# Kernel optimization log

Measured on AMD Instinct MI355X. Metric: run time of the kernel, lower is better.

The kernel has to match this reference:

```python
import jax, jax.numpy as jnp
import numpy as np

B, T, D = 8, 8192, 256
H = 16            # history_length
K = 3             # neighbor kernel_size
DECAY = 0.9
EPS = 1e-5


def _layernorm(x, g, b):
    m = jnp.mean(x, axis=-1, keepdims=True)
    v = jnp.var(x, axis=-1, keepdims=True)
    return (x - m) * jax.lax.rsqrt(v + EPS) * g + b


def _window_weighted_sum(x_pad, weights, seq_len):
    # sum_j w[j] * x_pad[:, j:j+T, :] -- fixed-weight local aggregation,
    # avoids materializing the [B,T,W,D] unfold tensor.
    out = weights[0] * x_pad[:, 0:seq_len, :]
    for j in range(1, weights.shape[0]):
        out = out + weights[j] * x_pad[:, j:j + seq_len, :]
    return out


def temporal_weights():
    w = DECAY ** np.arange(H, dtype=np.float32)
    return jnp.asarray(w / w.sum())


def setup_inputs() -> dict:
    key = jax.random.key(0)
    ks = jax.random.split(key, 16)
    s = 1.0 / np.sqrt(D)
    s2 = 1.0 / np.sqrt(2 * D)
    inp = {
        "x": jax.random.normal(ks[0], (B, T, D), jnp.float32),
        # LayerNorms
        "n1_g": jnp.ones((D,), jnp.float32), "n1_b": jnp.zeros((D,), jnp.float32),
        "n2_g": jnp.ones((D,), jnp.float32), "n2_b": jnp.zeros((D,), jnp.float32),
        "n3_g": jnp.ones((D,), jnp.float32), "n3_b": jnp.zeros((D,), jnp.float32),
        # temporal value/out proj (stored as [in,out])
        "t_Wv": jax.random.uniform(ks[1], (D, D), jnp.float32, -s, s),
        "t_bv": jax.random.uniform(ks[2], (D,), jnp.float32, -s, s),
        "t_Wo": jax.random.uniform(ks[3], (D, D), jnp.float32, -s, s),
        "t_bo": jax.random.uniform(ks[4], (D,), jnp.float32, -s, s),
        # neighbor value/out proj
        "a_Wv": jax.random.uniform(ks[5], (D, D), jnp.float32, -s, s),
        "a_bv": jax.random.uniform(ks[6], (D,), jnp.float32, -s, s),
        "a_Wo": jax.random.uniform(ks[7], (D, D), jnp.float32, -s, s),
        "a_bo": jax.random.uniform(ks[8], (D,), jnp.float32, -s, s),
        # FFN
        "f_W1": jax.random.uniform(ks[9], (D, 2 * D), jnp.float32, -s, s),
        "f_b1": jax.random.uniform(ks[10], (2 * D,), jnp.float32, -s, s),
        "f_W2": jax.random.uniform(ks[11], (2 * D, D), jnp.float32, -s2, s2),
        "f_b2": jax.random.uniform(ks[12], (D,), jnp.float32, -s2, s2),
    }
    return inp


def reference(x, n1_g, n1_b, n2_g, n2_b, n3_g, n3_b,
              t_Wv, t_bv, t_Wo, t_bo,
              a_Wv, a_bv, a_Wo, a_bo,
              f_W1, f_b1, f_W2, f_b2):
    # --- temporal memory: causal fixed exponential-decay window ---
    h = _layernorm(x, n1_g, n1_b)
    h_pad = jnp.pad(h, ((0, 0), (H - 1, 0), (0, 0)))  # zeros on the left
    tw = temporal_weights()  # tw[j] weights the j-th-oldest element (decay^j)
    agg = _window_weighted_sum(h_pad, tw, T)
    # weights sum to 1 => weighted-sum-of-linear == linear-of-weighted-sum
    attended = agg @ t_Wv + t_bv
    x = x + (attended @ t_Wo + t_bo)

    # --- neighbor attention: [t-1, t, t+1] uniform window, replicate pad ---
    h = _layernorm(x, n2_g, n2_b)
    h_pad = jnp.pad(h, ((0, 0), (1, 1), (0, 0)), mode="edge")
    nw = jnp.full((K,), 1.0 / K, jnp.float32)
    agg = _window_weighted_sum(h_pad, nw, T)
    attended = agg @ a_Wv + a_bv
    x = x + (attended @ a_Wo + a_bo)

    # --- FFN (dropout is identity at eval) ---
    h = _layernorm(x, n3_g, n3_b)
    h = jax.nn.gelu(h @ f_W1 + f_b1, approximate=False)
    x = x + (h @ f_W2 + f_b2)
    return x
```

## Files before the change

kernel.cpp:

```cpp
#include <hip/hip_runtime.h>
#include <cstdint>
#include <cstddef>

#define TT 8192
#define BB 8
#define DD 256
#define NTOK (BB * TT)

typedef unsigned short u16;
typedef unsigned int u32;

typedef __attribute__((ext_vector_type(8))) short bf16x8;
typedef __attribute__((ext_vector_type(4))) float f32x4;

__device__ __forceinline__ float bf2f(u16 u) {
    u32 v = ((u32)u) << 16;
    float f;
    __builtin_memcpy(&f, &v, 4);
    return f;
}

__device__ __forceinline__ u16 f2bf(float f) {
    u32 v;
    __builtin_memcpy(&v, &f, 4);
    u32 r = (v + 0x7FFFu + ((v >> 16) & 1u)) >> 16;
    return (u16)r;
}

__device__ __forceinline__ uint2 pack4(const float* v) {
    uint2 p;
    p.x = (u32)f2bf(v[0]) | ((u32)f2bf(v[1]) << 16);
    p.y = (u32)f2bf(v[2]) | ((u32)f2bf(v[3]) << 16);
    return p;
}

__device__ __forceinline__ void unpack4(uint2 p, float* v) {
    v[0] = bf2f((u16)(p.x & 0xFFFFu));
    v[1] = bf2f((u16)(p.x >> 16));
    v[2] = bf2f((u16)(p.y & 0xFFFFu));
    v[3] = bf2f((u16)(p.y >> 16));
}

__device__ __forceinline__ uint4 pack8(const float* v) {
    uint4 p;
    p.x = (u32)f2bf(v[0]) | ((u32)f2bf(v[1]) << 16);
    p.y = (u32)f2bf(v[2]) | ((u32)f2bf(v[3]) << 16);
    p.z = (u32)f2bf(v[4]) | ((u32)f2bf(v[5]) << 16);
    p.w = (u32)f2bf(v[6]) | ((u32)f2bf(v[7]) << 16);
    return p;
}

__device__ __forceinline__ void unpack8(uint4 p, float* v) {
    v[0] = bf2f((u16)(p.x & 0xFFFFu));
    v[1] = bf2f((u16)(p.x >> 16));
    v[2] = bf2f((u16)(p.y & 0xFFFFu));
    v[3] = bf2f((u16)(p.y >> 16));
    v[4] = bf2f((u16)(p.z & 0xFFFFu));
    v[5] = bf2f((u16)(p.z >> 16));
    v[6] = bf2f((u16)(p.w & 0xFFFFu));
    v[7] = bf2f((u16)(p.w >> 16));
}

__global__ __launch_bounds__(256) void k_diag(float* out, float code) {
    out[(size_t)blockIdx.x * 256 + threadIdx.x] = code;
}

__global__ __launch_bounds__(256) void k_transpose(
    const float* s0, const float* s1, const float* s2, const float* s3,
    const float* s4, const float* s5,
    u16* d0, u16* d1, u16* d2, u16* d3, u16* d4, u16* d5) {
    const int z = blockIdx.z;
    const float* src;
    u16* dst;
    int K, N, tr;
    switch (z) {
        case 0: src = s0; dst = d0; K = 256; N = 256; tr = 1; break;
        case 1: src = s1; dst = d1; K = 256; N = 256; tr = 1; break;
        case 2: src = s2; dst = d2; K = 256; N = 512; tr = 1; break;
        case 3: src = s3; dst = d3; K = 512; N = 256; tr = 1; break;
        case 4: src = s4; dst = d4; K = 256; N = 256; tr = 0; break;
        default: src = s5; dst = d5; K = 256; N = 256; tr = 0; break;
    }
    const int nb = blockIdx.x * 32, kb = blockIdx.y * 32;
    if (nb >= N || kb >= K) return;
    const int tx = threadIdx.x & 31, ty = threadIdx.x >> 5;
    if (!tr) {
        for (int i = ty; i < 32; i += 8)
            dst[(size_t)(kb + i) * N + nb + tx] =
                f2bf(src[(size_t)(kb + i) * N + nb + tx]);
        return;
    }
    __shared__ u16 tile[32][33];
    for (int i = ty; i < 32; i += 8)
        tile[i][tx] = f2bf(src[(size_t)(kb + i) * N + nb + tx]);
    __syncthreads();
    for (int i = ty; i < 32; i += 8)
        dst[(size_t)(nb + i) * K + kb + tx] = tile[tx][i];
}

__global__ __launch_bounds__(256) void k_bias_compose(
    const float* tbv, const float* tWo, const float* tbo,
    const float* abv, const float* aWo, const float* abo,
    float* bc1, float* bc2) {
    const float* bv = blockIdx.x ? abv : tbv;
    const float* Wo = blockIdx.x ? aWo : tWo;
    const float* bo = blockIdx.x ? abo : tbo;
    float* bc = blockIdx.x ? bc2 : bc1;
    const int n = threadIdx.x;
    float s = bo[n];
    for (int j = 0; j < 256; j++) s += bv[j] * Wo[j * 256 + n];
    bc[n] = s;
}

__global__ __launch_bounds__(256) void k_ln_temporal(
    const float* __restrict__ x, const float* __restrict__ gw,
    const float* __restrict__ bw, u16* __restrict__ out) {
    const int b = blockIdx.y;
    const int t0 = blockIdx.x * 64;
    const int tid = threadIdx.x;
    const int wv = tid >> 6, lane = tid & 63;
    const int d4 = lane * 4;
    __shared__ u16 hl[79 * 256];

    const float4 gv = *(const float4*)(gw + d4);
    const float4 bv = *(const float4*)(bw + d4);

    for (int i = wv; i < 79; i += 4) {
        const int t = t0 + i - 15;
        if (t < 0) {
            *(uint2*)(hl + i * 256 + d4) = make_uint2(0u, 0u);
            continue;
        }
        const float4 v = *(const float4*)(x + ((size_t)b * TT + t) * DD + d4);
        float s = v.x + v.y + v.z + v.w;
        float ss = v.x * v.x + v.y * v.y + v.z * v.z + v.w * v.w;
        for (int m = 1; m < 64; m <<= 1) {
            s += __shfl_xor(s, m);
            ss += __shfl_xor(ss, m);
        }
        const float mean = s * (1.0f / 256.0f);
        const float var = ss * (1.0f / 256.0f) - mean * mean;
        const float rs = rsqrtf(fmaxf(var, 0.f) + 1e-5f);
        float h[4] = {(v.x - mean) * rs * gv.x + bv.x,
                      (v.y - mean) * rs * gv.y + bv.y,
                      (v.z - mean) * rs * gv.z + bv.z,
                      (v.w - mean) * rs * gv.w + bv.w};
        *(uint2*)(hl + i * 256 + d4) = pack4(h);
    }
    __syncthreads();

    float tw[16];
    {
        float p = 1.f, s = 0.f;
        for (int j = 0; j < 16; j++) {
            tw[j] = p;
            s += p;
            p *= 0.9f;
        }
        const float inv = 1.f / s;
        for (int j = 0; j < 16; j++) tw[j] *= inv;
    }
    const int dc = (tid & 63) * 4;
    const int tg = (tid >> 6) * 16;
    for (int ot = tg; ot < tg + 16; ++ot) {
        float a[4] = {0.f, 0.f, 0.f, 0.f};
        for (int j = 0; j < 16; j++) {
            float h[4];
            unpack4(*(const uint2*)(hl + (ot + j) * 256 + dc), h);
            a[0] += tw[j] * h[0];
            a[1] += tw[j] * h[1];
            a[2] += tw[j] * h[2];
            a[3] += tw[j] * h[3];
        }
        *(uint2*)(out + ((size_t)b * TT + t0 + ot) * DD + dc) = pack4(a);
    }
}

__global__ __launch_bounds__(256) void k_gemm_prep(
    const u16* __restrict__ A, const u16* __restrict__ Wt,
    u16* out, int M, int K, int Nc, int ldw) {
    const int m0 = blockIdx.y * 128;
    const int n0 = blockIdx.x * 128;
    const int tid = threadIdx.x;
    const int wv = tid >> 6, lane = tid & 63;
    const int quad = lane >> 4, l16 = lane & 15;
    const int wm = (wv >> 1) * 64, wn = (wv & 1) * 64;

    __shared__ u16 lA[128 * 40];
    __shared__ u16 lB[128 * 40];

    f32x4 acc[4][4];
#pragma unroll
    for (int i = 0; i < 4; i++)
#pragma unroll
        for (int j = 0; j < 4; j++) acc[i][j] = (f32x4){0.f, 0.f, 0.f, 0.f};

    const int r = tid >> 2;
    const int c = tid & 3;

    for (int k0 = 0; k0 < K; k0 += 32) {
        __syncthreads();
        {
            const uint4 a0 = *(const uint4*)(A + (size_t)(m0 + r) * K + k0 + c * 8);
            const uint4 a1 = *(const uint4*)(A + (size_t)(m0 + r + 64) * K + k0 + c * 8);
            const uint4 b0 = *(const uint4*)(Wt + (size_t)(n0 + r) * ldw + k0 + c * 8);
            const uint4 b1 = *(const uint4*)(Wt + (size_t)(n0 + r + 64) * ldw + k0 + c * 8);
            *(uint4*)(lA + r * 40 + c * 8) = a0;
            *(uint4*)(lA + (r + 64) * 40 + c * 8) = a1;
            *(uint4*)(lB + r * 40 + c * 8) = b0;
            *(uint4*)(lB + (r + 64) * 40 + c * 8) = b1;
        }
        __syncthreads();
        bf16x8 af[4], bfr[4];
#pragma unroll
        for (int i = 0; i < 4; i++)
            af[i] = *(const bf16x8*)(lA + (wm + i * 16 + l16) * 40 + quad * 8);
#pragma unroll
        for (int j = 0; j < 4; j++)
            bfr[j] = *(const bf16x8*)(lB + (wn + j * 16 + l16) * 40 + quad * 8);
#pragma unroll
        for (int i = 0; i < 4; i++)
#pragma unroll
            for (int j = 0; j < 4; j++)
                acc[i][j] = __builtin_amdgcn_mfma_f32_16x16x32_bf16(
                    af[i], bfr[j], acc[i][j], 0, 0, 0);
    }

#pragma unroll
    for (int i = 0; i < 4; i++) {
        const int rowb = m0 + wm + i * 16 + quad * 4;
#pragma unroll
        for (int j = 0; j < 4; j++) {
            const int col = n0 + wn + j * 16 + l16;
#pragma unroll
            for (int rr = 0; rr < 4; rr++)
                out[(size_t)(rowb + rr) * Nc + col] = f2bf(acc[i][j][rr]);
        }
    }
}

template <int AMODE>
__global__ __launch_bounds__(256) void k_mega2(
    const u16* __restrict__ A,
    const u16* __restrict__ Wt,
    const float* __restrict__ bias,
    const float* res,
    float* outf,
    const float* __restrict__ lng, const float* __restrict__ lnb,
    u16* __restrict__ hout) {
    const int m0 = blockIdx.x * 64;
    const int t = threadIdx.x;
    const int lane = t & 63, wv = t >> 6;
    const int quad = lane >> 4, l16 = lane & 15;
    const int wn = wv * 64;

    __shared__ u16 sA[8 * 64 * 40];
    float* sE = (float*)sA;
    __shared__ float sMean[16], sRstd[16];
    __shared__ float sG[256], sBl[256];

    sG[t] = lng[t];
    sBl[t] = lnb[t];

#pragma unroll
    for (int q = 0; q < 8; q++) {
        const int id = q * 256 + t;
        const int arow = id >> 5;
        const int c8 = (id & 31) * 8;
        const int ks = c8 >> 5;
        const int kc = c8 & 31;
        const int gr = m0 + arow;
        if (AMODE == 0) {
            *(uint4*)(sA + (ks * 64 + arow) * 40 + kc) =
                *(const uint4*)(A + (size_t)gr * 256 + c8);
        } else {
            const int rm = ((gr & (TT - 1)) == 0) ? gr : gr - 1;
            const int rp = (((gr + 1) & (TT - 1)) == 0) ? gr : gr + 1;
            float v0[8], v1[8], v2[8], o[8];
            unpack8(*(const uint4*)(A + (size_t)rm * 256 + c8), v0);
            unpack8(*(const uint4*)(A + (size_t)gr * 256 + c8), v1);
            unpack8(*(const uint4*)(A + (size_t)rp * 256 + c8), v2);
#pragma unroll
            for (int e = 0; e < 8; e++)
                o[e] = (v0[e] + v1[e] + v2[e]) * (1.0f / 3.0f);
            *(uint4*)(sA + (ks * 64 + arow) * 40 + kc) = pack8(o);
        }
    }

    f32x4 acc[4][4];
#pragma unroll
    for (int i = 0; i < 4; i++)
#pragma unroll
        for (int j = 0; j < 4; j++) acc[i][j] = (f32x4){0.f, 0.f, 0.f, 0.f};

    __syncthreads();

#pragma unroll
    for (int ks = 0; ks < 8; ks++) {
        bf16x8 bfr[4], af[4];
#pragma unroll
        for (int j = 0; j < 4; j++)
            bfr[j] = *(const bf16x8*)(Wt + (size_t)(wn + j * 16 + l16) * 256 +
                                      ks * 32 + quad * 8);
#pragma unroll
        for (int i = 0; i < 4; i++)
            af[i] = *(const bf16x8*)(sA + (ks * 64 + i * 16 + l16) * 40 +
                                     quad * 8);
#pragma unroll
        for (int i = 0; i < 4; i++)
#pragma unroll
            for (int j = 0; j < 4; j++)
                acc[i][j] = __builtin_amdgcn_mfma_f32_16x16x32_bf16(
                    af[i], bfr[j], acc[i][j], 0, 0, 0);
    }

    float bvl[4];
#pragma unroll
    for (int j = 0; j < 4; j++) bvl[j] = bias[wn + j * 16 + l16];

    const int row = t >> 4;
    const int colb = (t & 15) * 16;
    for (int cch = 0; cch < 4; cch++) {
        const int gr = m0 + cch * 16 + row;
        __syncthreads();
        {
            const float* rp = res + (size_t)gr * 256 + colb;
            float* sp = sE + row * 268 + colb;
#pragma unroll
            for (int q = 0; q < 4; q++)
                *(float4*)(sp + q * 4) = *(const float4*)(rp + q * 4);
        }
        __syncthreads();
#pragma unroll
        for (int j = 0; j < 4; j++) {
#pragma unroll
            for (int rr = 0; rr < 4; rr++) {
                const int rl = quad * 4 + rr;
                const int ad = rl * 268 + wn + j * 16 + l16;
                sE[ad] += acc[cch][j][rr] + bvl[j];
            }
        }
        __syncthreads();
#pragma unroll
        for (int r4 = 0; r4 < 4; r4++) {
            const int rl = wv * 4 + r4;
            const float4 vv = *(const float4*)(sE + rl * 268 + lane * 4);
            float s = vv.x + vv.y + vv.z + vv.w;
            float ss = vv.x * vv.x + vv.y * vv.y + vv.z * vv.z + vv.w * vv.w;
            for (int m = 1; m < 64; m <<= 1) {
                s += __shfl_xor(s, m);
                ss += __shfl_xor(ss, m);
            }
            if (lane == 0) {
                const float mean = s * (1.0f / 256.0f);
                const float var = ss * (1.0f / 256.0f) - mean * mean;
                sMean[rl] = mean;
                sRstd[rl] = rsqrtf(fmaxf(var, 0.f) + 1e-5f);
            }
        }
        __syncthreads();
        const float* sp = sE + row * 268 + colb;
        {
            float* op = outf + (size_t)gr * 256 + colb;
#pragma unroll
            for (int q = 0; q < 4; q++)
                *(float4*)(op + q * 4) = *(const float4*)(sp + q * 4);
        }
        {
            const float m = sMean[row], rs = sRstd[row];
            float h[16];
#pragma unroll
            for (int e = 0; e < 16; e++)
                h[e] = (sp[e] - m) * rs * sG[colb + e] + sBl[colb + e];
            u16* hp = hout + (size_t)gr * 256 + colb;
            *(uint4*)hp = pack8(h);
            *(uint4*)(hp + 8) = pack8(h + 8);
        }
    }
}

__global__ __launch_bounds__(256) void k_ffn(
    const u16* __restrict__ A,
    const u16* __restrict__ W1T,
    const float* __restrict__ b1,
    const u16* __restrict__ W2T,
    const float* __restrict__ b2,
    const float* res,
    float* out) {
    const int m0 = blockIdx.x * 64;
    const int t = threadIdx.x;
    const int lane = t & 63, wv = t >> 6;
    const int quad = lane >> 4, l16 = lane & 15;

    __shared__ u16 sA[8 * 64 * 40];
    __shared__ u16 sT[64 * 72];
    float* sE = (float*)sA;

#pragma unroll
    for (int q = 0; q < 8; q++) {
        const int id = q * 256 + t;
        const int arow = id >> 5;
        const int c8 = (id & 31) * 8;
        const int ks = c8 >> 5;
        const int kc = c8 & 31;
        *(uint4*)(sA + (ks * 64 + arow) * 40 + kc) =
            *(const uint4*)(A + (size_t)(m0 + arow) * 256 + c8);
    }

    f32x4 acc2[4][4];
#pragma unroll
    for (int i = 0; i < 4; i++)
#pragma unroll
        for (int jj = 0; jj < 4; jj++) acc2[i][jj] = (f32x4){0.f, 0.f, 0.f, 0.f};

    __syncthreads();

    for (int j = 0; j < 8; j++) {
        bf16x8 bw2[8];
#pragma unroll
        for (int kh = 0; kh < 2; kh++)
#pragma unroll
            for (int jj = 0; jj < 4; jj++)
                bw2[kh * 4 + jj] = *(const bf16x8*)(
                    W2T + (size_t)(wv * 64 + jj * 16 + l16) * 512 + j * 64 +
                    kh * 32 + quad * 8);
        const int n1 = j * 64 + wv * 16 + l16;
        bf16x8 bw[8];
#pragma unroll
        for (int ks = 0; ks < 8; ks++)
            bw[ks] = *(const bf16x8*)(W1T + (size_t)n1 * 256 + ks * 32 + quad * 8);
        f32x4 acc1[4];
#pragma unroll
        for (int i = 0; i < 4; i++) acc1[i] = (f32x4){0.f, 0.f, 0.f, 0.f};
#pragma unroll
        for (int ks = 0; ks < 8; ks++) {
#pragma unroll
            for (int i = 0; i < 4; i++) {
                const bf16x8 af = *(const bf16x8*)(
                    sA + (ks * 64 + i * 16 + l16) * 40 + quad * 8);
                acc1[i] = __builtin_amdgcn_mfma_f32_16x16x32_bf16(
                    af, bw[ks], acc1[i], 0, 0, 0);
            }
        }
        const float b1l = b1[n1];
#pragma unroll
        for (int i = 0; i < 4; i++)
#pragma unroll
            for (int rr = 0; rr < 4; rr++) {
                float v = acc1[i][rr] + b1l;
                v = 0.5f * v * (1.0f + erff(v * 0.70710678118654752f));
                sT[(i * 16 + quad * 4 + rr) * 72 + wv * 16 + l16] = f2bf(v);
            }
        __syncthreads();
#pragma unroll
        for (int kh = 0; kh < 2; kh++) {
#pragma unroll
            for (int i = 0; i < 4; i++) {
                const bf16x8 af = *(const bf16x8*)(
                    sT + (i * 16 + l16) * 72 + kh * 32 + quad * 8);
#pragma unroll
                for (int jj = 0; jj < 4; jj++)
                    acc2[i][jj] = __builtin_amdgcn_mfma_f32_16x16x32_bf16(
                        af, bw2[kh * 4 + jj], acc2[i][jj], 0, 0, 0);
            }
        }
        __syncthreads();
    }

    float bvl[4];
#pragma unroll
    for (int jj = 0; jj < 4; jj++) bvl[jj] = b2[wv * 64 + jj * 16 + l16];
    const int row = t >> 4;
    const int colb = (t & 15) * 16;
    for (int cch = 0; cch < 4; cch++) {
        const int gr = m0 + cch * 16 + row;
        __syncthreads();
        {
            const float* rp = res + (size_t)gr * 256 + colb;
            float* sp = sE + row * 268 + colb;
#pragma unroll
            for (int q = 0; q < 4; q++)
                *(float4*)(sp + q * 4) = *(const float4*)(rp + q * 4);
        }
        __syncthreads();
#pragma unroll
        for (int jj = 0; jj < 4; jj++)
#pragma unroll
            for (int rr = 0; rr < 4; rr++) {
                const int ad = (quad * 4 + rr) * 268 + wv * 64 + jj * 16 + l16;
                sE[ad] += acc2[cch][jj][rr] + bvl[jj];
            }
        __syncthreads();
        {
            float* op = out + (size_t)gr * 256 + colb;
            const float* sp = sE + row * 268 + colb;
#pragma unroll
            for (int q = 0; q < 4; q++)
                *(float4*)(op + q * 4) = *(const float4*)(sp + q * 4);
        }
    }
}

extern "C" void kernel_launch(void* const* d_in, const int* in_sizes, int n_in,
                              void* d_out, int out_size, void* d_ws,
                              size_t ws_size, hipStream_t stream) {
    const float* x = (const float*)d_in[0];
    const float* n1g = (const float*)d_in[1];
    const float* n1b = (const float*)d_in[2];
    const float* n2g = (const float*)d_in[3];
    const float* n2b = (const float*)d_in[4];
    const float* n3g = (const float*)d_in[5];
    const float* n3b = (const float*)d_in[6];
    const float* tWv = (const float*)d_in[7];
    const float* tbv = (const float*)d_in[8];
    const float* tWo = (const float*)d_in[9];
    const float* tbo = (const float*)d_in[10];
    const float* aWv = (const float*)d_in[11];
    const float* abv = (const float*)d_in[12];
    const float* aWo = (const float*)d_in[13];
    const float* abo = (const float*)d_in[14];
    const float* fW1 = (const float*)d_in[15];
    const float* fb1 = (const float*)d_in[16];
    const float* fW2 = (const float*)d_in[17];
    const float* fb2 = (const float*)d_in[18];
    float* outp = (float*)d_out;

    u16* wq = (u16*)d_ws;
    u16* tWoT = wq;
    u16* aWoT = wq + 65536;
    u16* fW1T = wq + 131072;
    u16* fW2T = wq + 262144;
    u16* WcT1 = wq + 393216;
    u16* WcT2 = wq + 458752;
    u16* tWvB = wq + 524288;
    u16* aWvB = wq + 589824;
    float* bc1 = (float*)(wq + 655360);
    float* bc2 = (float*)(wq + 655872);
    const size_t W_ELEMS = 656384;
    const size_t SLOT = (size_t)NTOK * 256;
    u16* slot1 = wq + W_ELEMS;
    u16* slot2 = slot1 + SLOT;
    u16* slot3 = slot2 + SLOT;

    const size_t need = (W_ELEMS + 3 * SLOT) * 2;
    if (ws_size < need) {
        k_diag<<<dim3(NTOK), 256, 0, stream>>>(outp,
                                               512.0f + (float)(ws_size >> 20));
        return;
    }

    k_transpose<<<dim3(16, 16, 6), 256, 0, stream>>>(
        tWo, aWo, fW1, fW2, tWv, aWv, tWoT, aWoT, fW1T, fW2T, tWvB, aWvB);
    k_gemm_prep<<<dim3(2, 2), 256, 0, stream>>>(tWoT, tWvB, WcT1, 256, 256,
                                                256, 256);
    k_gemm_prep<<<dim3(2, 2), 256, 0, stream>>>(aWoT, aWvB, WcT2, 256, 256,
                                                256, 256);
    k_bias_compose<<<dim3(2), 256, 0, stream>>>(tbv, tWo, tbo, abv, aWo, abo,
                                                bc1, bc2);

    const dim3 mg(NTOK / 64);

    k_ln_temporal<<<dim3(TT / 64, BB), 256, 0, stream>>>(x, n1g, n1b, slot1);

    k_mega2<0><<<mg, 256, 0, stream>>>(slot1, WcT1, bc1, x, outp, n2g, n2b,
                                       slot2);

    k_mega2<1><<<mg, 256, 0, stream>>>(slot2, WcT2, bc2, outp, outp, n3g, n3b,
                                       slot1);

    k_ffn<<<mg, 256, 0, stream>>>(slot1, fW1T, fb1, fW2T, fb2, outp, outp);
}
```

Baseline: 399.9 us.

## Fuse LN1 temporal aggregation with composed projection GEMM and LN2

Merges the LN1 + temporal-decay window kernel with the following composed Wv·Wo GEMM, residual add and LN2 into a single kernel. The aggregated tile now stays in shared memory instead of round-tripping through a bf16 global buffer, and one kernel launch is removed. In exchange the fused kernel uses more LDS (79x256 halo plus a 64x264 tile), which may lower occupancy. It also reads B fragments straight from global memory rather than staging them in LDS.

```diff
diff --git a/kernel.cpp b/kernel.cpp
--- a/kernel.cpp
+++ b/kernel.cpp
@@ -112,70 +112,6 @@
     bc[n] = s;
 }
 
-__global__ __launch_bounds__(256) void k_ln_temporal(
-    const float* __restrict__ x, const float* __restrict__ gw,
-    const float* __restrict__ bw, u16* __restrict__ out) {
-    const int b = blockIdx.y;
-    const int t0 = blockIdx.x * 64;
-    const int tid = threadIdx.x;
-    const int wv = tid >> 6, lane = tid & 63;
-    const int d4 = lane * 4;
-    __shared__ u16 hl[79 * 256];
-
-    const float4 gv = *(const float4*)(gw + d4);
-    const float4 bv = *(const float4*)(bw + d4);
-
-    for (int i = wv; i < 79; i += 4) {
-        const int t = t0 + i - 15;
-        if (t < 0) {
-            *(uint2*)(hl + i * 256 + d4) = make_uint2(0u, 0u);
-            continue;
-        }
-        const float4 v = *(const float4*)(x + ((size_t)b * TT + t) * DD + d4);
-        float s = v.x + v.y + v.z + v.w;
-        float ss = v.x * v.x + v.y * v.y + v.z * v.z + v.w * v.w;
-        for (int m = 1; m < 64; m <<= 1) {
-            s += __shfl_xor(s, m);
-            ss += __shfl_xor(ss, m);
-        }
-        const float mean = s * (1.0f / 256.0f);
-        const float var = ss * (1.0f / 256.0f) - mean * mean;
-        const float rs = rsqrtf(fmaxf(var, 0.f) + 1e-5f);
-        float h[4] = {(v.x - mean) * rs * gv.x + bv.x,
-                      (v.y - mean) * rs * gv.y + bv.y,
-                      (v.z - mean) * rs * gv.z + bv.z,
-                      (v.w - mean) * rs * gv.w + bv.w};
-        *(uint2*)(hl + i * 256 + d4) = pack4(h);
-    }
-    __syncthreads();
-
-    float tw[16];
-    {
-        float p = 1.f, s = 0.f;
-        for (int j = 0; j < 16; j++) {
-            tw[j] = p;
-            s += p;
-            p *= 0.9f;
-        }
-        const float inv = 1.f / s;
-        for (int j = 0; j < 16; j++) tw[j] *= inv;
-    }
-    const int dc = (tid & 63) * 4;
-    const int tg = (tid >> 6) * 16;
-    for (int ot = tg; ot < tg + 16; ++ot) {
-        float a[4] = {0.f, 0.f, 0.f, 0.f};
-        for (int j = 0; j < 16; j++) {
-            float h[4];
-            unpack4(*(const uint2*)(hl + (ot + j) * 256 + dc), h);
-            a[0] += tw[j] * h[0];
-            a[1] += tw[j] * h[1];
-            a[2] += tw[j] * h[2];
-            a[3] += tw[j] * h[3];
-        }
-        *(uint2*)(out + ((size_t)b * TT + t0 + ot) * DD + dc) = pack4(a);
-    }
-}
-
 __global__ __launch_bounds__(256) void k_gemm_prep(
     const u16* __restrict__ A, const u16* __restrict__ Wt,
     u16* out, int M, int K, int Nc, int ldw) {
@@ -235,6 +171,173 @@
 #pragma unroll
             for (int rr = 0; rr < 4; rr++)
                 out[(size_t)(rowb + rr) * Nc + col] = f2bf(acc[i][j][rr]);
+        }
+    }
+}
+
+__global__ __launch_bounds__(256) void k_p12(
+    const float* __restrict__ x, const float* __restrict__ n1g,
+    const float* __restrict__ n1b, const u16* __restrict__ Wt,
+    const float* __restrict__ bias, float* outf,
+    const float* __restrict__ lng, const float* __restrict__ lnb,
+    u16* __restrict__ hout) {
+    const int b = blockIdx.y;
+    const int t0 = blockIdx.x * 64;
+    const size_t base = (size_t)b * TT;
+    const int t = threadIdx.x;
+    const int lane = t & 63, wv = t >> 6;
+    const int quad = lane >> 4, l16 = lane & 15;
+    const int wn = wv * 64;
+
+    __shared__ __attribute__((aligned(16))) u16 hl[79 * 256];
+    __shared__ __attribute__((aligned(16))) u16 sAg[64 * 264];
+    float* sE = (float*)hl;
+    __shared__ float sMean[16], sRstd[16];
+    __shared__ float sG[256], sBl[256];
+
+    sG[t] = lng[t];
+    sBl[t] = lnb[t];
+
+    const int d4 = lane * 4;
+    {
+        const float4 gv = *(const float4*)(n1g + d4);
+        const float4 bv = *(const float4*)(n1b + d4);
+        for (int i = wv; i < 79; i += 4) {
+            const int tt = t0 + i - 15;
+            if (tt < 0) {
+                *(uint2*)(hl + i * 256 + d4) = make_uint2(0u, 0u);
+                continue;
+            }
+            const float4 v = *(const float4*)(x + (base + tt) * DD + d4);
+            float s = v.x + v.y + v.z + v.w;
+            float ss = v.x * v.x + v.y * v.y + v.z * v.z + v.w * v.w;
+            for (int m = 1; m < 64; m <<= 1) {
+                s += __shfl_xor(s, m);
+                ss += __shfl_xor(ss, m);
+            }
+            const float mean = s * (1.0f / 256.0f);
+            const float var = ss * (1.0f / 256.0f) - mean * mean;
+            const float rs = rsqrtf(fmaxf(var, 0.f) + 1e-5f);
+            float h[4] = {(v.x - mean) * rs * gv.x + bv.x,
+                          (v.y - mean) * rs * gv.y + bv.y,
+                          (v.z - mean) * rs * gv.z + bv.z,
+                          (v.w - mean) * rs * gv.w + bv.w};
+            *(uint2*)(hl + i * 256 + d4) = pack4(h);
+        }
+    }
+    __syncthreads();
+
+    {
+        float tw[16];
+        float p = 1.f, s = 0.f;
+        for (int j = 0; j < 16; j++) {
+            tw[j] = p;
+            s += p;
+            p *= 0.9f;
+        }
+        const float inv = 1.f / s;
+        for (int j = 0; j < 16; j++) tw[j] *= inv;
+        const int tg = wv * 16;
+        for (int ot = tg; ot < tg + 16; ++ot) {
+            float a[4] = {0.f, 0.f, 0.f, 0.f};
+            for (int j = 0; j < 16; j++) {
+                float h[4];
+                unpack4(*(const uint2*)(hl + (ot + j) * 256 + d4), h);
+                a[0] += tw[j] * h[0];
+                a[1] += tw[j] * h[1];
+                a[2] += tw[j] * h[2];
+                a[3] += tw[j] * h[3];
+            }
+            *(uint2*)(sAg + ot * 264 + d4) = pack4(a);
+        }
+    }
+    __syncthreads();
+
+    f32x4 acc[4][4];
+#pragma unroll
+    for (int i = 0; i < 4; i++)
+#pragma unroll
+        for (int j = 0; j < 4; j++) acc[i][j] = (f32x4){0.f, 0.f, 0.f, 0.f};
+#pragma unroll
+    for (int ks = 0; ks < 8; ks++) {
+        bf16x8 bfr[4], af[4];
+#pragma unroll
+        for (int j = 0; j < 4; j++)
+            bfr[j] = *(const bf16x8*)(Wt + (size_t)(wn + j * 16 + l16) * 256 +
+                                      ks * 32 + quad * 8);
+#pragma unroll
+        for (int i = 0; i < 4; i++)
+            af[i] = *(const bf16x8*)(sAg + (i * 16 + l16) * 264 + ks * 32 +
+                                     quad * 8);
+#pragma unroll
+        for (int i = 0; i < 4; i++)
+#pragma unroll
+            for (int j = 0; j < 4; j++)
+                acc[i][j] = __builtin_amdgcn_mfma_f32_16x16x32_bf16(
+                    af[i], bfr[j], acc[i][j], 0, 0, 0);
+    }
+
+    float bvl[4];
+#pragma unroll
+    for (int j = 0; j < 4; j++) bvl[j] = bias[wn + j * 16 + l16];
+
+    const int row = t >> 4;
+    const int colb = (t & 15) * 16;
+    for (int cch = 0; cch < 4; cch++) {
+        const size_t grow = base + t0 + cch * 16 + row;
+        __syncthreads();
+        {
+            const float* rp = x + grow * 256 + colb;
+            float* sp = sE + row * 268 + colb;
+#pragma unroll
+            for (int q = 0; q < 4; q++)
+                *(float4*)(sp + q * 4) = *(const float4*)(rp + q * 4);
+        }
+        __syncthreads();
+#pragma unroll
+        for (int j = 0; j < 4; j++) {
+#pragma unroll
+            for (int rr = 0; rr < 4; rr++) {
+                const int rl = quad * 4 + rr;
+                const int ad = rl * 268 + wn + j * 16 + l16;
+                sE[ad] += acc[cch][j][rr] + bvl[j];
+            }
+        }
+        __syncthreads();
+#pragma unroll
+        for (int r4 = 0; r4 < 4; r4++) {
+            const int rl = wv * 4 + r4;
+            const float4 vv = *(const float4*)(sE + rl * 268 + lane * 4);
+            float s = vv.x + vv.y + vv.z + vv.w;
+            float ss = vv.x * vv.x + vv.y * vv.y + vv.z * vv.z + vv.w * vv.w;
+            for (int m = 1; m < 64; m <<= 1) {
+                s += __shfl_xor(s, m);
+                ss += __shfl_xor(ss, m);
+            }
+            if (lane == 0) {
+                const float mean = s * (1.0f / 256.0f);
+                const float var = ss * (1.0f / 256.0f) - mean * mean;
+                sMean[rl] = mean;
+                sRstd[rl] = rsqrtf(fmaxf(var, 0.f) + 1e-5f);
+            }
+        }
+        __syncthreads();
+        const float* sp = sE + row * 268 + colb;
+        {
+            float* op = outf + grow * 256 + colb;
+#pragma unroll
+            for (int q = 0; q < 4; q++)
+                *(float4*)(op + q * 4) = *(const float4*)(sp + q * 4);
+        }
+        {
+            const float m = sMean[row], rs = sRstd[row];
+            float h[16];
+#pragma unroll
+            for (int e = 0; e < 16; e++)
+                h[e] = (sp[e] - m) * rs * sG[colb + e] + sBl[colb + e];
+            u16* hp = hout + grow * 256 + colb;
+            *(uint4*)hp = pack8(h);
+            *(uint4*)(hp + 8) = pack8(h + 8);
         }
     }
 }
@@ -254,7 +357,7 @@
     const int quad = lane >> 4, l16 = lane & 15;
     const int wn = wv * 64;
 
-    __shared__ u16 sA[8 * 64 * 40];
+    __shared__ __attribute__((aligned(16))) u16 sA[8 * 64 * 40];
     float* sE = (float*)sA;
     __shared__ float sMean[16], sRstd[16];
     __shared__ float sG[256], sBl[256];
@@ -392,8 +495,8 @@
     const int lane = t & 63, wv = t >> 6;
     const int quad = lane >> 4, l16 = lane & 15;
 
-    __shared__ u16 sA[8 * 64 * 40];
-    __shared__ u16 sT[64 * 72];
+    __shared__ __attribute__((aligned(16))) u16 sA[8 * 64 * 40];
+    __shared__ __attribute__((aligned(16))) u16 sT[64 * 72];
     float* sE = (float*)sA;
 
 #pragma unroll
@@ -541,6 +644,7 @@
     u16* slot1 = wq + W_ELEMS;
     u16* slot2 = slot1 + SLOT;
     u16* slot3 = slot2 + SLOT;
+    (void)slot3;
 
     const size_t need = (W_ELEMS + 3 * SLOT) * 2;
     if (ws_size < need) {
@@ -560,10 +664,8 @@
 
     const dim3 mg(NTOK / 64);
 
-    k_ln_temporal<<<dim3(TT / 64, BB), 256, 0, stream>>>(x, n1g, n1b, slot1);
-
-    k_mega2<0><<<mg, 256, 0, stream>>>(slot1, WcT1, bc1, x, outp, n2g, n2b,
-                                       slot2);
+    k_p12<<<dim3(TT / 64, BB), 256, 0, stream>>>(x, n1g, n1b, WcT1, bc1, outp,
+                                                 n2g, n2b, slot2);
 
     k_mega2<1><<<mg, 256, 0, stream>>>(slot2, WcT2, bc2, outp, outp, n3g, n3b,
                                        slot1);
```

Measured after the change: 399.0 us. No clear change (-0.2%).
